# Kernel optimization log

Measured on AMD Instinct MI355X. Metric: run time of the kernel, lower is better.

## Reference

```python
import jax, jax.numpy as jnp
import numpy as np

D = 128
L_SIZE = 65536
C_SIZE = 32768
E = 262144
N_ITERS = 4


def _mlp(x, w1, b1, w2, b2):
    # 2-layer satbench MLP: Linear -> relu -> Linear
    return jax.nn.relu(x @ w1 + b1) @ w2 + b2


def setup_inputs() -> dict:
    key = jax.random.key(0)
    ks = iter(jax.random.split(key, 32))

    def lin(fi, fo):
        # torch nn.Linear default init, stored as (in, out)
        bound = 1.0 / np.sqrt(fi)
        w = jax.random.uniform(next(ks), (fi, fo), minval=-bound, maxval=bound, dtype=jnp.float32)
        b = jax.random.uniform(next(ks), (fo,), minval=-bound, maxval=bound, dtype=jnp.float32)
        return w, b

    s = np.sqrt(2.0 / D).astype(np.float32)
    inp = {}
    inp['l_edge_index'] = jax.random.randint(next(ks), (E,), 0, L_SIZE, dtype=jnp.int64)
    inp['c_edge_index'] = jax.random.randint(next(ks), (E,), 0, C_SIZE, dtype=jnp.int64)
    inp['l_init'] = jax.random.normal(next(ks), (1, D), dtype=jnp.float32) * s
    inp['c_init'] = jax.random.normal(next(ks), (1, D), dtype=jnp.float32) * s
    inp['w_l2c1'], inp['b_l2c1'] = lin(D, D)
    inp['w_l2c2'], inp['b_l2c2'] = lin(D, D)
    inp['w_c2l1'], inp['b_c2l1'] = lin(D, D)
    inp['w_c2l2'], inp['b_c2l2'] = lin(D, D)
    inp['w_l2l1'], inp['b_l2l1'] = lin(D, D)
    inp['w_l2l2'], inp['b_l2l2'] = lin(D, D)
    inp['w_cu'], inp['b_cu'] = lin(2 * D, D)
    inp['w_lu'], inp['b_lu'] = lin(3 * D, D)
    inp['l_size'] = L_SIZE
    inp['c_size'] = C_SIZE
    return inp


def reference(l_edge_index, c_edge_index, l_init, c_init,
              w_l2c1, b_l2c1, w_l2c2, b_l2c2,
              w_c2l1, b_c2l1, w_c2l2, b_c2l2,
              w_l2l1, b_l2l1, w_l2l2, b_l2l2,
              w_cu, b_cu, w_lu, b_lu, l_size, c_size):
    d = l_init.shape[1]
    ones = jnp.ones((l_edge_index.shape[0], 1), dtype=l_init.dtype)
    l_deg = jax.ops.segment_sum(ones, l_edge_index, num_segments=l_size)   # (L,1)
    c_deg = jax.ops.segment_sum(ones, c_edge_index, num_segments=c_size)   # (C,1)
    degree_norm = jnp.sqrt(l_deg[l_edge_index]) * jnp.sqrt(c_deg[c_edge_index])  # (E,1)

    l_emb = jnp.tile(l_init, (l_size, 1))  # (L,d)
    c_emb = jnp.tile(c_init, (c_size, 1))  # (C,d)

    def step(carry, _):
        l_emb, c_emb = carry
        l2c_msg = _mlp(l_emb, w_l2c1, b_l2c1, w_l2c2, b_l2c2)[l_edge_index]  # (E,d)
        c2l_msg = _mlp(c_emb, w_c2l1, b_c2l1, w_c2l2, b_c2l2)[c_edge_index]  # (E,d)
        # swap positive/negative literal partner embeddings (pairs are adjacent rows)
        l2l_in = l_emb.reshape(l_size // 2, 2, d)[:, ::-1, :].reshape(l_size, d)
        l2l_msg = _mlp(l2l_in, w_l2l1, b_l2l1, w_l2l2, b_l2l2)              # (L,d)
        l2c_aggr = jax.ops.segment_sum(l2c_msg / degree_norm, c_edge_index, num_segments=c_size)
        c_new = jnp.concatenate([c_emb, l2c_aggr], axis=1) @ w_cu + b_cu
        c2l_aggr = jax.ops.segment_sum(c2l_msg / degree_norm, l_edge_index, num_segments=l_size)
        l_new = jnp.concatenate([l_emb, c2l_aggr, l2l_msg], axis=1) @ w_lu + b_lu
        return (l_new, c_new), None

    (l_emb, c_emb), _ = jax.lax.scan(step, (l_emb, c_emb), None, length=N_ITERS)
    return l_emb
```

## Files before the change

### kernel.cpp

```cpp
#include <hip/hip_runtime.h>
#include <hip/hip_bf16.h>

#define D_ 128
#define L_ 65536
#define C_ 32768
#define E_ 262144

typedef __hip_bfloat16 bf16;
typedef __attribute__((ext_vector_type(8))) short short8;
typedef __attribute__((ext_vector_type(4))) float f32x4;

__global__ void detect_k(const unsigned short* __restrict__ wmem,
                         const int* __restrict__ li, int* __restrict__ flags) {
    int t = blockIdx.x * 512 + threadIdx.x;
    if (t < 8192) {
        unsigned short h = wmem[2 * t];
        float v = __bfloat162float(*(const bf16*)&h);
        if (!(fabsf(v) < 0.5f)) atomicOr(&flags[0], 1);
    }
    if (t < 2048) {
        if (li[2 * t + 1] != 0) atomicOr(&flags[1], 1);
    }
}

__device__ __forceinline__ void split2(float v, unsigned short& h, unsigned short& l) {
    bf16 bh = __float2bfloat16(v);
    float fh = __bfloat162float(bh);
    bf16 bl = __float2bfloat16(v - fh);
    h = *(unsigned short*)&bh;
    l = *(unsigned short*)&bl;
}

__device__ __forceinline__ float ldf(const void* s, int i, int isf32) {
    return isf32 ? ((const float*)s)[i] : __bfloat162float(((const bf16*)s)[i]);
}

__global__ void fixdeg_k(const int* __restrict__ ls, const int* __restrict__ cs,
                         int* __restrict__ ld_idx, int* __restrict__ cd_idx,
                         int* __restrict__ ldeg, int* __restrict__ cdeg,
                         const int* __restrict__ flags) {
    int i = blockIdx.x * 256 + threadIdx.x;
    int is32 = flags[1];
    if (i < E_) {
        int v = is32 ? ls[i] : ls[2 * i];
        v = min(max(v, 0), L_ - 1);
        ld_idx[i] = v;
        atomicAdd(&ldeg[v], 1);
    } else {
        int j = i - E_;
        int v = is32 ? cs[j] : cs[2 * j];
        v = min(max(v, 0), C_ - 1);
        cd_idx[j] = v;
        atomicAdd(&cdeg[v], 1);
    }
}

__global__ void cvtwb_k(const void* s0, const void* s1, const void* s2, const void* s3,
                        const void* s4, const void* s5, const void* s6, const void* s7,
                        const void* t0, const void* t1, const void* t2, const void* t3,
                        const void* t4, const void* t5, const void* t6, const void* t7,
                        unsigned short* __restrict__ hi, unsigned short* __restrict__ lo,
                        float* __restrict__ bb, const int* __restrict__ flags) {
    int i = blockIdx.x * 256 + threadIdx.x;
    int isf = flags[0];
    if (i >= 180224) {
        int j = i - 180224;
        const void* src;
        switch (j >> 7) {
            case 0: src = t0; break; case 1: src = t1; break;
            case 2: src = t2; break; case 3: src = t3; break;
            case 4: src = t4; break; case 5: src = t5; break;
            case 6: src = t6; break; default: src = t7; break;
        }
        bb[j] = ldf(src, j & 127, isf);
        return;
    }
    const void* src; int K, base;
    if      (i <  16384) { src = s0; K = 128; base = 0; }
    else if (i <  32768) { src = s1; K = 128; base = 16384; }
    else if (i <  49152) { src = s2; K = 128; base = 32768; }
    else if (i <  65536) { src = s3; K = 128; base = 49152; }
    else if (i <  81920) { src = s4; K = 128; base = 65536; }
    else if (i <  98304) { src = s5; K = 128; base = 81920; }
    else if (i < 131072) { src = s6; K = 256; base = 98304; }
    else                 { src = s7; K = 384; base = 131072; }
    int e = i - base;
    int k = e >> 7, n = e & 127;
    float v = ldf(src, e, isf);
    unsigned short h, l;
    split2(v, h, l);
    hi[base + n * K + k] = h;
    lo[base + n * K + k] = l;
}

__global__ void init2_k(const void* __restrict__ lv, const void* __restrict__ cv,
                        float* __restrict__ lemb, float* __restrict__ cemb,
                        const int* __restrict__ flags) {
    int i4 = blockIdx.x * 256 + threadIdx.x;
    int isf = flags[0];
    const void* src; float* dst; int o;
    if (i4 < L_ * 32) { src = lv; dst = lemb; o = i4; }
    else              { src = cv; dst = cemb; o = i4 - L_ * 32; }
    int j = (o & 31) * 4;
    float4 v;
    v.x = ldf(src, j + 0, isf);
    v.y = ldf(src, j + 1, isf);
    v.z = ldf(src, j + 2, isf);
    v.w = ldf(src, j + 3, isf);
    ((float4*)dst)[o] = v;
}

__global__ void scan1b_k(const int* __restrict__ ldeg, const int* __restrict__ cdeg,
                         int* __restrict__ lout, int* __restrict__ cout,
                         int* __restrict__ bsumL, int* __restrict__ bsumC) {
    __shared__ int s[256];
    const int* in; int* out; int* bs; int tile;
    if (blockIdx.x < 256) { in = ldeg; out = lout; bs = bsumL; tile = blockIdx.x; }
    else                  { in = cdeg; out = cout; bs = bsumC; tile = blockIdx.x - 256; }
    int i = tile * 256 + threadIdx.x;
    int v = in[i];
    s[threadIdx.x] = v;
    __syncthreads();
#pragma unroll
    for (int off = 1; off < 256; off <<= 1) {
        int t = (threadIdx.x >= off) ? s[threadIdx.x - off] : 0;
        __syncthreads();
        s[threadIdx.x] += t;
        __syncthreads();
    }
    out[i] = s[threadIdx.x] - v;
    if (threadIdx.x == 255) bs[tile] = s[255];
}

__global__ void scan2b_k(int* __restrict__ bL, int* __restrict__ bC) {
    __shared__ int s[256];
    int* b = blockIdx.x ? bC : bL;
    int nb = blockIdx.x ? 128 : 256;
    int v = (threadIdx.x < nb) ? b[threadIdx.x] : 0;
    s[threadIdx.x] = v;
    __syncthreads();
#pragma unroll
    for (int off = 1; off < 256; off <<= 1) {
        int t = (threadIdx.x >= off) ? s[threadIdx.x - off] : 0;
        __syncthreads();
        s[threadIdx.x] += t;
        __syncthreads();
    }
    if (threadIdx.x < nb) b[threadIdx.x] = s[threadIdx.x] - v;
}

__global__ void scan3b_k(int* __restrict__ lptr, int* __restrict__ cptr,
                         const int* __restrict__ bsumL, const int* __restrict__ bsumC,
                         int* __restrict__ lcur, int* __restrict__ ccur,
                         const int* __restrict__ ldeg, const int* __restrict__ cdeg,
                         float* __restrict__ invsq_l, float* __restrict__ invsq_c) {
    int b = blockIdx.x, t = threadIdx.x;
    if (b < 256) {
        int i = b * 256 + t;
        int v = lptr[i] + bsumL[b];
        lptr[i] = v; lcur[i] = v;
        int d = ldeg[i];
        invsq_l[i] = d ? rsqrtf((float)d) : 0.0f;
    } else {
        int i = (b - 256) * 256 + t;
        int v = cptr[i] + bsumC[b - 256];
        cptr[i] = v; ccur[i] = v;
        int d = cdeg[i];
        invsq_c[i] = d ? rsqrtf((float)d) : 0.0f;
    }
}

__global__ void place_k(const int* __restrict__ li, const int* __restrict__ ci,
                        int* __restrict__ lcur, int* __restrict__ ccur,
                        int* __restrict__ l_other, int* __restrict__ c_other) {
    int e = blockIdx.x * 256 + threadIdx.x;
    if (e >= E_) return;
    int l = li[e], c = ci[e];
    int p = atomicAdd(&ccur[c], 1);
    c_other[p] = l;
    int q = atomicAdd(&lcur[l], 1);
    l_other[q] = c;
}

__global__ __launch_bounds__(256) void gather2_k(
    const int* __restrict__ cptr, const int* __restrict__ cdeg, const int* __restrict__ c_other,
    const unsigned int* __restrict__ lmsg, const float* __restrict__ invsq_c, float* __restrict__ caggr,
    const int* __restrict__ lptr, const int* __restrict__ ldeg, const int* __restrict__ l_other,
    const unsigned int* __restrict__ cmsg, const float* __restrict__ invsq_l, float* __restrict__ laggr,
    int nC) {
    int node = (blockIdx.x * 256 + threadIdx.x) >> 6;
    int lane = threadIdx.x & 63;
    bool cside = node < nC;
    int j = cside ? node : node - nC;
    const int* ptr = cside ? cptr : lptr;
    const int* dg  = cside ? cdeg : ldeg;
    const int* oth = cside ? c_other : l_other;
    const unsigned int* msg = cside ? lmsg : cmsg;
    float sc = (cside ? invsq_c : invsq_l)[j];
    float* out = cside ? caggr : laggr;
    int s = ptr[j], cnt = dg[j];
    float2 a0 = {0.f, 0.f}, a1 = {0.f, 0.f};
    int k = 0;
    for (; k + 4 <= cnt; k += 4) {
        int o0 = oth[s + k], o1 = oth[s + k + 1], o2 = oth[s + k + 2], o3 = oth[s + k + 3];
        unsigned int u0 = msg[(size_t)o0 * 64 + lane];
        unsigned int u1 = msg[(size_t)o1 * 64 + lane];
        unsigned int u2 = msg[(size_t)o2 * 64 + lane];
        unsigned int u3 = msg[(size_t)o3 * 64 + lane];
        a0.x += __uint_as_float(u0 << 16) + __uint_as_float(u2 << 16);
        a0.y += __uint_as_float(u0 & 0xffff0000u) + __uint_as_float(u2 & 0xffff0000u);
        a1.x += __uint_as_float(u1 << 16) + __uint_as_float(u3 << 16);
        a1.y += __uint_as_float(u1 & 0xffff0000u) + __uint_as_float(u3 & 0xffff0000u);
    }
    for (; k < cnt; k++) {
        int o = oth[s + k];
        unsigned int u = msg[(size_t)o * 64 + lane];
        a0.x += __uint_as_float(u << 16);
        a0.y += __uint_as_float(u & 0xffff0000u);
    }
    a0.x = (a0.x + a1.x) * sc;
    a0.y = (a0.y + a1.y) * sc;
    *(float2*)&out[(size_t)j * D_ + 2 * lane] = a0;
}

__global__ __launch_bounds__(256, 2) void mlp3_k(
    const float* __restrict__ l_cur, const float* __restrict__ c_cur,
    const unsigned short* __restrict__ wt_hi, const unsigned short* __restrict__ wt_lo,
    const float* __restrict__ bb,
    const float* __restrict__ invsq_l, const float* __restrict__ invsq_c,
    bf16* __restrict__ l_msg, bf16* __restrict__ c_msg, bf16* __restrict__ l2lb,
    int nL, int nC) {
    __shared__ char smem[66048];
    unsigned short (*a_hi)[40] = (unsigned short(*)[40])(smem);
    unsigned short (*a_lo)[40] = (unsigned short(*)[40])(smem + 10240);
    unsigned short (*b_hi)[40] = (unsigned short(*)[40])(smem + 20480);
    unsigned short (*b_lo)[40] = (unsigned short(*)[40])(smem + 30720);
    unsigned short* h_hi = (unsigned short*)(smem);
    unsigned short* h_lo = (unsigned short*)(smem + 32768);
    float* scv = (float*)(smem + 65536);

    int b = blockIdx.x, seg, tile;
    if (b < nL)           { seg = 0; tile = b; }
    else if (b < nL + nC) { seg = 1; tile = b - nL; }
    else                  { seg = 2; tile = b - nL - nC; }
    const float* A = (seg == 1) ? c_cur : l_cur;
    bf16* outp = (seg == 0) ? l_msg : (seg == 1) ? c_msg : l2lb;
    const float* invsq = (seg == 0) ? invsq_l : (seg == 1) ? invsq_c : nullptr;
    const unsigned short* W1h = wt_hi + seg * 32768;
    const unsigned short* W1l = wt_lo + seg * 32768;
    const unsigned short* W2h = W1h + 16384;
    const unsigned short* W2l = W1l + 16384;
    const float* b1v = bb + seg * 256;
    const float* b2v = b1v + 128;
    const int swap = (seg == 2);

    const int t = threadIdx.x;
    const int br0 = tile * 128;
    const int w = t >> 6, lane = t & 63;
    const int wr = w >> 1, wc = w & 1;
    const int quad = lane >> 4, cl = lane & 15;

    if (t < 128) scv[t] = invsq ? invsq[br0 + t] : 1.0f;

    f32x4 acc[4][4];
#pragma unroll
    for (int i = 0; i < 4; i++)
#pragma unroll
        for (int j = 0; j < 4; j++) acc[i][j] = (f32x4){0.f, 0.f, 0.f, 0.f};

    for (int kt = 0; kt < 128; kt += 32) {
#pragma unroll
        for (int i = 0; i < 4; i++) {
            int f = t + 256 * i;
            int r = f >> 3, kq = f & 7;
            int gr = br0 + r;
            if (swap) gr ^= 1;
            const float4 v = *(const float4*)&A[(size_t)gr * D_ + kt + 4 * kq];
            unsigned short h0, l0, h1, l1, h2, l2, h3, l3;
            split2(v.x, h0, l0); split2(v.y, h1, l1);
            split2(v.z, h2, l2); split2(v.w, h3, l3);
            *(ushort4*)&a_hi[r][4 * kq] = make_ushort4(h0, h1, h2, h3);
            *(ushort4*)&a_lo[r][4 * kq] = make_ushort4(l0, l1, l2, l3);
            *(ushort4*)&b_hi[r][4 * kq] = *(const ushort4*)&W1h[(size_t)r * 128 + kt + 4 * kq];
            *(ushort4*)&b_lo[r][4 * kq] = *(const ushort4*)&W1l[(size_t)r * 128 + kt + 4 * kq];
        }
        __syncthreads();
        short8 af_h[4], af_l[4];
#pragma unroll
        for (int i = 0; i < 4; i++) {
            int row = 64 * wr + 16 * i + cl;
            af_h[i] = *(const short8*)&a_hi[row][quad * 8];
            af_l[i] = *(const short8*)&a_lo[row][quad * 8];
        }
#pragma unroll
        for (int j = 0; j < 4; j++) {
            int col = 64 * wc + 16 * j + cl;
            short8 bf_h = *(const short8*)&b_hi[col][quad * 8];
            short8 bf_l = *(const short8*)&b_lo[col][quad * 8];
#pragma unroll
            for (int i = 0; i < 4; i++) {
                acc[i][j] = __builtin_amdgcn_mfma_f32_16x16x32_bf16(af_h[i], bf_h, acc[i][j], 0, 0, 0);
                acc[i][j] = __builtin_amdgcn_mfma_f32_16x16x32_bf16(af_h[i], bf_l, acc[i][j], 0, 0, 0);
                acc[i][j] = __builtin_amdgcn_mfma_f32_16x16x32_bf16(af_l[i], bf_h, acc[i][j], 0, 0, 0);
            }
        }
        __syncthreads();
    }
#pragma unroll
    for (int j = 0; j < 4; j++) {
        int col = 64 * wc + 16 * j + cl;
        float bv = b1v[col];
        int g = col >> 3, go = col & 7;
#pragma unroll
        for (int i = 0; i < 4; i++) {
            int rloc = 64 * wr + 16 * i + quad * 4;
#pragma unroll
            for (int rg = 0; rg < 4; rg++) {
                float v = fmaxf(acc[i][j][rg] + bv, 0.0f);
                unsigned short hh, ll;
                split2(v, hh, ll);
                int r = rloc + rg;
                int off = r * 128 + ((g ^ (r & 15)) << 3) + go;
                h_hi[off] = hh;
                h_lo[off] = ll;
            }
        }
    }
    __syncthreads();
#pragma unroll
    for (int i = 0; i < 4; i++)
#pragma unroll
        for (int j = 0; j < 4; j++) acc[i][j] = (f32x4){0.f, 0.f, 0.f, 0.f};

    for (int kt = 0; kt < 128; kt += 32) {
        short8 af_h[4], af_l[4];
        int gbase = (kt >> 3) + quad;
#pragma unroll
        for (int i = 0; i < 4; i++) {
            int r = 64 * wr + 16 * i + cl;
            int off = r * 128 + ((gbase ^ cl) << 3);
            af_h[i] = *(const short8*)&h_hi[off];
            af_l[i] = *(const short8*)&h_lo[off];
        }
#pragma unroll
        for (int j = 0; j < 4; j++) {
            int col = 64 * wc + 16 * j + cl;
            const short8 bf_h = *(const short8*)&W2h[(size_t)col * 128 + kt + quad * 8];
            const short8 bf_l = *(const short8*)&W2l[(size_t)col * 128 + kt + quad * 8];
#pragma unroll
            for (int i = 0; i < 4; i++) {
                acc[i][j] = __builtin_amdgcn_mfma_f32_16x16x32_bf16(af_h[i], bf_h, acc[i][j], 0, 0, 0);
                acc[i][j] = __builtin_amdgcn_mfma_f32_16x16x32_bf16(af_h[i], bf_l, acc[i][j], 0, 0, 0);
                acc[i][j] = __builtin_amdgcn_mfma_f32_16x16x32_bf16(af_l[i], bf_h, acc[i][j], 0, 0, 0);
            }
        }
    }
#pragma unroll
    for (int j = 0; j < 4; j++) {
        int col = 64 * wc + 16 * j + cl;
        float bv = b2v[col];
#pragma unroll
        for (int i = 0; i < 4; i++) {
            int rloc = 64 * wr + 16 * i + quad * 4;
#pragma unroll
            for (int rg = 0; rg < 4; rg++)
                outp[(size_t)(br0 + rloc + rg) * D_ + col] =
                    __float2bfloat16((acc[i][j][rg] + bv) * scv[rloc + rg]);
        }
    }
}

template <int FINAL>
__global__ __launch_bounds__(256, 2) void update_k(
    const float* __restrict__ l_cur, const float* __restrict__ c_cur,
    const float* __restrict__ laggr, const float* __restrict__ caggr,
    const bf16* __restrict__ l2lb,
    const unsigned short* __restrict__ wt_hi, const unsigned short* __restrict__ wt_lo,
    const float* __restrict__ bb,
    float* __restrict__ c_nxt, float* __restrict__ l_nxt,
    void* __restrict__ dout, const int* __restrict__ flags) {
    __shared__ unsigned short a_hi[128][40], a_lo[128][40];
    __shared__ unsigned short b_hi[128][40], b_lo[128][40];
    const int t = threadIdx.x;
    int b = blockIdx.x;
    const bool cseg = (!FINAL) && (b < 256);
    const int tile = (FINAL || cseg) ? b : b - 256;
    const int K = cseg ? 256 : 384;
    const float* A0 = cseg ? c_cur : l_cur;
    const float* A1 = cseg ? caggr : laggr;
    const unsigned short* Wh = wt_hi + (cseg ? 98304 : 131072);
    const unsigned short* Wl = wt_lo + (cseg ? 98304 : 131072);
    const float* bias = bb + (cseg ? 768 : 896);
    const int br0 = tile * 128;
    const int w = t >> 6, lane = t & 63;
    const int wr = w >> 1, wc = w & 1;
    const int quad = lane >> 4, cl = lane & 15;

    f32x4 acc[4][4];
#pragma unroll
    for (int i = 0; i < 4; i++)
#pragma unroll
        for (int j = 0; j < 4; j++) acc[i][j] = (f32x4){0.f, 0.f, 0.f, 0.f};

    for (int kt = 0; kt < K; kt += 32) {
        const bool haslo = (kt < 256);
        const int koff = kt & 127;
#pragma unroll
        for (int i = 0; i < 4; i++) {
            int f = t + 256 * i;
            int r = f >> 3, kq = f & 7;
            if (haslo) {
                const float* As = (kt < 128) ? A0 : A1;
                const float4 v = *(const float4*)&As[(size_t)(br0 + r) * D_ + koff + 4 * kq];
                unsigned short h0, l0, h1, l1, h2, l2, h3, l3;
                split2(v.x, h0, l0); split2(v.y, h1, l1);
                split2(v.z, h2, l2); split2(v.w, h3, l3);
                *(ushort4*)&a_hi[r][4 * kq] = make_ushort4(h0, h1, h2, h3);
                *(ushort4*)&a_lo[r][4 * kq] = make_ushort4(l0, l1, l2, l3);
            } else {
                *(ushort4*)&a_hi[r][4 * kq] =
                    *(const ushort4*)&l2lb[(size_t)(br0 + r) * D_ + koff + 4 * kq];
            }
            *(ushort4*)&b_hi[r][4 * kq] = *(const ushort4*)&Wh[(size_t)r * K + kt + 4 * kq];
            *(ushort4*)&b_lo[r][4 * kq] = *(const ushort4*)&Wl[(size_t)r * K + kt + 4 * kq];
        }
        __syncthreads();
        short8 af_h[4], af_l[4];
#pragma unroll
        for (int i = 0; i < 4; i++) {
            int row = 64 * wr + 16 * i + cl;
            af_h[i] = *(const short8*)&a_hi[row][quad * 8];
            if (haslo) af_l[i] = *(const short8*)&a_lo[row][quad * 8];
        }
#pragma unroll
        for (int j = 0; j < 4; j++) {
            int col = 64 * wc + 16 * j + cl;
            short8 bf_h = *(const short8*)&b_hi[col][quad * 8];
            short8 bf_l = *(const short8*)&b_lo[col][quad * 8];
#pragma unroll
            for (int i = 0; i < 4; i++) {
                acc[i][j] = __builtin_amdgcn_mfma_f32_16x16x32_bf16(af_h[i], bf_h, acc[i][j], 0, 0, 0);
                acc[i][j] = __builtin_amdgcn_mfma_f32_16x16x32_bf16(af_h[i], bf_l, acc[i][j], 0, 0, 0);
                if (haslo)
                    acc[i][j] = __builtin_amdgcn_mfma_f32_16x16x32_bf16(af_l[i], bf_h, acc[i][j], 0, 0, 0);
            }
        }
        __syncthreads();
    }
    const int f32out = FINAL ? flags[0] : 1;
#pragma unroll
    for (int j = 0; j < 4; j++) {
        int col = 64 * wc + 16 * j + cl;
        float bv = bias[col];
#pragma unroll
        for (int i = 0; i < 4; i++) {
            int rbase = br0 + 64 * wr + 16 * i + quad * 4;
#pragma unroll
            for (int rg = 0; rg < 4; rg++) {
                float v = acc[i][j][rg] + bv;
                size_t idx = (size_t)(rbase + rg) * D_ + col;
                if (FINAL) {
                    if (f32out) ((float*)dout)[idx] = v;
                    else        ((bf16*)dout)[idx] = __float2bfloat16(v);
                } else {
                    (cseg ? c_nxt : l_nxt)[idx] = v;
                }
            }
        }
    }
}

extern "C" void kernel_launch(void* const* d_in, const int* in_sizes, int n_in,
                              void* d_out, int out_size, void* d_ws, size_t ws_size,
                              hipStream_t stream) {
    const int* li_raw = (const int*)d_in[0];
    const int* ci_raw = (const int*)d_in[1];

    float* ws = (float*)d_ws;
    float* lbuf0 = ws;
    float* lbuf1 = lbuf0 + (size_t)L_ * D_;
    float* l2lb  = lbuf1 + (size_t)L_ * D_;
    float* laggr = l2lb + (size_t)L_ * D_;
    float* cbuf0 = laggr + (size_t)L_ * D_;
    float* cbuf1 = cbuf0 + (size_t)C_ * D_;
    float* caggr = cbuf1 + (size_t)C_ * D_;
    float* invsq_l = caggr + (size_t)C_ * D_;
    float* invsq_c = invsq_l + L_;
    float* bb    = invsq_c + C_;
    unsigned short* wt_hi = (unsigned short*)(bb + 1024);
    unsigned short* wt_lo = wt_hi + 180224;
    int*   li    = (int*)(wt_lo + 180224);
    int*   ci    = li + E_;
    int*   l_other = ci + E_;
    int*   c_other = l_other + E_;
    int*   ldegi = c_other + E_;
    int*   cdegi = ldegi + L_;
    int*   lptr  = cdegi + C_;
    int*   cptr  = lptr + L_;
    int*   lcur  = cptr + C_;
    int*   ccur  = lcur + L_;
    int*   bsumL = ccur + C_;
    int*   bsumC = bsumL + 256;
    int*   flags = bsumC + 128;

    hipMemsetAsync(flags, 0, 2 * sizeof(int), stream);
    detect_k<<<16, 512, 0, stream>>>((const unsigned short*)d_in[4], li_raw, flags);

    hipMemsetAsync(ldegi, 0, (size_t)(L_ + C_) * sizeof(int), stream);
    fixdeg_k<<<2 * E_ / 256, 256, 0, stream>>>(li_raw, ci_raw, li, ci, ldegi, cdegi, flags);

    cvtwb_k<<<708, 256, 0, stream>>>(d_in[4], d_in[6], d_in[8], d_in[10], d_in[12],
                                     d_in[14], d_in[16], d_in[18],
                                     d_in[5], d_in[7], d_in[9], d_in[11], d_in[13],
                                     d_in[15], d_in[17], d_in[19], wt_hi, wt_lo, bb, flags);

    scan1b_k<<<384, 256, 0, stream>>>(ldegi, cdegi, lptr, cptr, bsumL, bsumC);
    scan2b_k<<<2, 256, 0, stream>>>(bsumL, bsumC);
    scan3b_k<<<384, 256, 0, stream>>>(lptr, cptr, bsumL, bsumC, lcur, ccur,
                                      ldegi, cdegi, invsq_l, invsq_c);
    place_k<<<E_ / 256, 256, 0, stream>>>(li, ci, lcur, ccur, l_other, c_other);

    init2_k<<<(L_ + C_) * 32 / 256, 256, 0, stream>>>(d_in[2], d_in[3], lbuf0, cbuf0, flags);

    float* l_cur = lbuf0; float* l_nxt = lbuf1;
    float* c_cur = cbuf0; float* c_nxt = cbuf1;

    const int nL = L_ / 128, nC = C_ / 128;
    for (int it = 0; it < 3; it++) {
        mlp3_k<<<2 * nL + nC, 256, 0, stream>>>(
            l_cur, c_cur, wt_hi, wt_lo, bb, invsq_l, invsq_c,
            (bf16*)l_nxt, (bf16*)c_nxt, (bf16*)l2lb, nL, nC);
        gather2_k<<<(C_ + L_) / 4, 256, 0, stream>>>(
            cptr, cdegi, c_other, (const unsigned int*)l_nxt, invsq_c, caggr,
            lptr, ldegi, l_other, (const unsigned int*)c_nxt, invsq_l, laggr, C_);
        update_k<0><<<768, 256, 0, stream>>>(
            l_cur, c_cur, laggr, caggr, (const bf16*)l2lb, wt_hi, wt_lo, bb,
            c_nxt, l_nxt, nullptr, flags);
        float* tmp = l_cur; l_cur = l_nxt; l_nxt = tmp;
        tmp = c_cur; c_cur = c_nxt; c_nxt = tmp;
    }
    mlp3_k<<<nC + nL, 256, 0, stream>>>(
        l_cur, c_cur, wt_hi, wt_lo, bb, invsq_l, invsq_c,
        (bf16*)l_nxt, (bf16*)c_nxt, (bf16*)l2lb, 0, nC);
    gather2_k<<<L_ / 4, 256, 0, stream>>>(
        cptr, cdegi, c_other, (const unsigned int*)l_nxt, invsq_c, caggr,
        lptr, ldegi, l_other, (const unsigned int*)c_nxt, invsq_l, laggr, 0);
    update_k<1><<<512, 256, 0, stream>>>(
        l_cur, c_cur, laggr, caggr, (const bf16*)l2lb, wt_hi, wt_lo, bb,
        nullptr, nullptr, d_out, flags);
}
```

Baseline: 692.7 us.

## Fuse l2c and l2l MLPs into one block sharing the staged literal tile

The MLP kernel now has each literal tile load and split its 128x128 fp32 activation block once into swizzled shared memory, then compute both the l2c and l2l first layers from it. The partner swap moves to the output side by writing l2l rows to index r^1. First-layer weights are read straight from global memory instead of being staged through LDS. This halves literal activation reads and the number of literal blocks, at the cost of more registers (two accumulator sets), which may limit occupancy.

```diff
diff --git a/kernel.cpp b/kernel.cpp
--- a/kernel.cpp
+++ b/kernel.cpp
@@ -9,6 +9,8 @@
 typedef __hip_bfloat16 bf16;
 typedef __attribute__((ext_vector_type(8))) short short8;
 typedef __attribute__((ext_vector_type(4))) float f32x4;
+
+__device__ __forceinline__ int uswz(int r) { return (r + (r >> 2)) & 3; }
 
 __global__ void detect_k(const unsigned short* __restrict__ wmem,
                          const int* __restrict__ li, int* __restrict__ flags) {
@@ -223,149 +225,243 @@
     *(float2*)&out[(size_t)j * D_ + 2 * lane] = a0;
 }
 
-__global__ __launch_bounds__(256, 2) void mlp3_k(
+__global__ __launch_bounds__(256, 2) void mlp3f_k(
     const float* __restrict__ l_cur, const float* __restrict__ c_cur,
     const unsigned short* __restrict__ wt_hi, const unsigned short* __restrict__ wt_lo,
     const float* __restrict__ bb,
     const float* __restrict__ invsq_l, const float* __restrict__ invsq_c,
     bf16* __restrict__ l_msg, bf16* __restrict__ c_msg, bf16* __restrict__ l2lb,
-    int nL, int nC) {
+    int nL, int fin) {
     __shared__ char smem[66048];
-    unsigned short (*a_hi)[40] = (unsigned short(*)[40])(smem);
-    unsigned short (*a_lo)[40] = (unsigned short(*)[40])(smem + 10240);
-    unsigned short (*b_hi)[40] = (unsigned short(*)[40])(smem + 20480);
-    unsigned short (*b_lo)[40] = (unsigned short(*)[40])(smem + 30720);
-    unsigned short* h_hi = (unsigned short*)(smem);
+    unsigned short* h_hi = (unsigned short*)smem;
     unsigned short* h_lo = (unsigned short*)(smem + 32768);
     float* scv = (float*)(smem + 65536);
 
-    int b = blockIdx.x, seg, tile;
-    if (b < nL)           { seg = 0; tile = b; }
-    else if (b < nL + nC) { seg = 1; tile = b - nL; }
-    else                  { seg = 2; tile = b - nL - nC; }
-    const float* A = (seg == 1) ? c_cur : l_cur;
-    bf16* outp = (seg == 0) ? l_msg : (seg == 1) ? c_msg : l2lb;
-    const float* invsq = (seg == 0) ? invsq_l : (seg == 1) ? invsq_c : nullptr;
-    const unsigned short* W1h = wt_hi + seg * 32768;
-    const unsigned short* W1l = wt_lo + seg * 32768;
+    const int b = blockIdx.x;
+    const bool lseg = (b < nL);
+    const int tile = lseg ? b : b - nL;
+    const int br0 = tile * 128;
+    const float* A = lseg ? l_cur : c_cur;
+    const int s1 = lseg ? 0 : 1;
+    const unsigned short* W1h = wt_hi + s1 * 32768;
+    const unsigned short* W1l = wt_lo + s1 * 32768;
     const unsigned short* W2h = W1h + 16384;
     const unsigned short* W2l = W1l + 16384;
-    const float* b1v = bb + seg * 256;
+    const unsigned short* V1h = wt_hi + 65536;
+    const unsigned short* V1l = wt_lo + 65536;
+    const unsigned short* V2h = V1h + 16384;
+    const unsigned short* V2l = V1l + 16384;
+    const float* b1v = bb + s1 * 256;
     const float* b2v = b1v + 128;
-    const int swap = (seg == 2);
+    const float* d1v = bb + 512;
+    const float* d2v = bb + 640;
+    bf16* out1 = lseg ? l_msg : c_msg;
+    const bool do1 = !(fin && lseg);
+    const bool do2 = lseg;
 
     const int t = threadIdx.x;
-    const int br0 = tile * 128;
     const int w = t >> 6, lane = t & 63;
     const int wr = w >> 1, wc = w & 1;
     const int quad = lane >> 4, cl = lane & 15;
 
-    if (t < 128) scv[t] = invsq ? invsq[br0 + t] : 1.0f;
-
-    f32x4 acc[4][4];
+    if (t < 128) scv[t] = (lseg ? invsq_l : invsq_c)[br0 + t];
+
+    {
+        float4 v[16];
+#pragma unroll
+        for (int c = 0; c < 16; c++) {
+            int f = t + 256 * c;
+            int r = f >> 5, kq = f & 31;
+            v[c] = *(const float4*)&A[(size_t)(br0 + r) * D_ + 4 * kq];
+        }
+#pragma unroll
+        for (int c = 0; c < 16; c++) {
+            int f = t + 256 * c;
+            int r = f >> 5, kq = f & 31;
+            int s = kq >> 3, kq2 = kq & 7;
+            unsigned short h0, l0, h1, l1, h2, l2, h3, l3;
+            split2(v[c].x, h0, l0); split2(v[c].y, h1, l1);
+            split2(v[c].z, h2, l2); split2(v[c].w, h3, l3);
+            int ga = s * 16384 + r * 64 + (((kq2 >> 1) ^ uswz(r)) << 4) + (kq2 & 1) * 8;
+            *(ushort4*)(smem + ga) = make_ushort4(h0, h1, h2, h3);
+            *(ushort4*)(smem + 8192 + ga) = make_ushort4(l0, l1, l2, l3);
+        }
+    }
+    __syncthreads();
+
+    f32x4 acc1[4][4], acc2[4][4];
 #pragma unroll
     for (int i = 0; i < 4; i++)
 #pragma unroll
-        for (int j = 0; j < 4; j++) acc[i][j] = (f32x4){0.f, 0.f, 0.f, 0.f};
-
-    for (int kt = 0; kt < 128; kt += 32) {
-#pragma unroll
-        for (int i = 0; i < 4; i++) {
-            int f = t + 256 * i;
-            int r = f >> 3, kq = f & 7;
-            int gr = br0 + r;
-            if (swap) gr ^= 1;
-            const float4 v = *(const float4*)&A[(size_t)gr * D_ + kt + 4 * kq];
-            unsigned short h0, l0, h1, l1, h2, l2, h3, l3;
-            split2(v.x, h0, l0); split2(v.y, h1, l1);
-            split2(v.z, h2, l2); split2(v.w, h3, l3);
-            *(ushort4*)&a_hi[r][4 * kq] = make_ushort4(h0, h1, h2, h3);
-            *(ushort4*)&a_lo[r][4 * kq] = make_ushort4(l0, l1, l2, l3);
-            *(ushort4*)&b_hi[r][4 * kq] = *(const ushort4*)&W1h[(size_t)r * 128 + kt + 4 * kq];
-            *(ushort4*)&b_lo[r][4 * kq] = *(const ushort4*)&W1l[(size_t)r * 128 + kt + 4 * kq];
-        }
-        __syncthreads();
+        for (int j = 0; j < 4; j++) {
+            acc1[i][j] = (f32x4){0.f, 0.f, 0.f, 0.f};
+            acc2[i][j] = (f32x4){0.f, 0.f, 0.f, 0.f};
+        }
+
+    for (int kt = 0; kt < 4; kt++) {
+        const char* base = smem + kt * 16384;
         short8 af_h[4], af_l[4];
 #pragma unroll
         for (int i = 0; i < 4; i++) {
             int row = 64 * wr + 16 * i + cl;
-            af_h[i] = *(const short8*)&a_hi[row][quad * 8];
-            af_l[i] = *(const short8*)&a_lo[row][quad * 8];
+            int so = row * 64 + ((quad ^ uswz(row)) << 4);
+            af_h[i] = *(const short8*)(base + so);
+            af_l[i] = *(const short8*)(base + 8192 + so);
         }
 #pragma unroll
         for (int j = 0; j < 4; j++) {
             int col = 64 * wc + 16 * j + cl;
-            short8 bf_h = *(const short8*)&b_hi[col][quad * 8];
-            short8 bf_l = *(const short8*)&b_lo[col][quad * 8];
-#pragma unroll
-            for (int i = 0; i < 4; i++) {
-                acc[i][j] = __builtin_amdgcn_mfma_f32_16x16x32_bf16(af_h[i], bf_h, acc[i][j], 0, 0, 0);
-                acc[i][j] = __builtin_amdgcn_mfma_f32_16x16x32_bf16(af_h[i], bf_l, acc[i][j], 0, 0, 0);
-                acc[i][j] = __builtin_amdgcn_mfma_f32_16x16x32_bf16(af_l[i], bf_h, acc[i][j], 0, 0, 0);
-            }
-        }
-        __syncthreads();
-    }
-#pragma unroll
-    for (int j = 0; j < 4; j++) {
-        int col = 64 * wc + 16 * j + cl;
-        float bv = b1v[col];
-        int g = col >> 3, go = col & 7;
-#pragma unroll
-        for (int i = 0; i < 4; i++) {
-            int rloc = 64 * wr + 16 * i + quad * 4;
-#pragma unroll
-            for (int rg = 0; rg < 4; rg++) {
-                float v = fmaxf(acc[i][j][rg] + bv, 0.0f);
-                unsigned short hh, ll;
-                split2(v, hh, ll);
-                int r = rloc + rg;
-                int off = r * 128 + ((g ^ (r & 15)) << 3) + go;
-                h_hi[off] = hh;
-                h_lo[off] = ll;
+            size_t wo = (size_t)col * 128 + kt * 32 + quad * 8;
+            if (do1) {
+                short8 bh = *(const short8*)&W1h[wo];
+                short8 bl = *(const short8*)&W1l[wo];
+#pragma unroll
+                for (int i = 0; i < 4; i++) {
+                    acc1[i][j] = __builtin_amdgcn_mfma_f32_16x16x32_bf16(af_h[i], bh, acc1[i][j], 0, 0, 0);
+                    acc1[i][j] = __builtin_amdgcn_mfma_f32_16x16x32_bf16(af_h[i], bl, acc1[i][j], 0, 0, 0);
+                    acc1[i][j] = __builtin_amdgcn_mfma_f32_16x16x32_bf16(af_l[i], bh, acc1[i][j], 0, 0, 0);
+                }
+            }
+            if (do2) {
+                short8 bh = *(const short8*)&V1h[wo];
+                short8 bl = *(const short8*)&V1l[wo];
+#pragma unroll
+                for (int i = 0; i < 4; i++) {
+                    acc2[i][j] = __builtin_amdgcn_mfma_f32_16x16x32_bf16(af_h[i], bh, acc2[i][j], 0, 0, 0);
+                    acc2[i][j] = __builtin_amdgcn_mfma_f32_16x16x32_bf16(af_h[i], bl, acc2[i][j], 0, 0, 0);
+                    acc2[i][j] = __builtin_amdgcn_mfma_f32_16x16x32_bf16(af_l[i], bh, acc2[i][j], 0, 0, 0);
+                }
             }
         }
     }
     __syncthreads();
-#pragma unroll
-    for (int i = 0; i < 4; i++)
-#pragma unroll
-        for (int j = 0; j < 4; j++) acc[i][j] = (f32x4){0.f, 0.f, 0.f, 0.f};
-
-    for (int kt = 0; kt < 128; kt += 32) {
-        short8 af_h[4], af_l[4];
-        int gbase = (kt >> 3) + quad;
-#pragma unroll
-        for (int i = 0; i < 4; i++) {
-            int r = 64 * wr + 16 * i + cl;
-            int off = r * 128 + ((gbase ^ cl) << 3);
-            af_h[i] = *(const short8*)&h_hi[off];
-            af_l[i] = *(const short8*)&h_lo[off];
-        }
+
+    if (do1) {
 #pragma unroll
         for (int j = 0; j < 4; j++) {
             int col = 64 * wc + 16 * j + cl;
-            const short8 bf_h = *(const short8*)&W2h[(size_t)col * 128 + kt + quad * 8];
-            const short8 bf_l = *(const short8*)&W2l[(size_t)col * 128 + kt + quad * 8];
+            float bv = b1v[col];
+            int g = col >> 3, go = col & 7;
 #pragma unroll
             for (int i = 0; i < 4; i++) {
-                acc[i][j] = __builtin_amdgcn_mfma_f32_16x16x32_bf16(af_h[i], bf_h, acc[i][j], 0, 0, 0);
-                acc[i][j] = __builtin_amdgcn_mfma_f32_16x16x32_bf16(af_h[i], bf_l, acc[i][j], 0, 0, 0);
-                acc[i][j] = __builtin_amdgcn_mfma_f32_16x16x32_bf16(af_l[i], bf_h, acc[i][j], 0, 0, 0);
-            }
-        }
-    }
-#pragma unroll
-    for (int j = 0; j < 4; j++) {
-        int col = 64 * wc + 16 * j + cl;
-        float bv = b2v[col];
-#pragma unroll
-        for (int i = 0; i < 4; i++) {
-            int rloc = 64 * wr + 16 * i + quad * 4;
-#pragma unroll
-            for (int rg = 0; rg < 4; rg++)
-                outp[(size_t)(br0 + rloc + rg) * D_ + col] =
-                    __float2bfloat16((acc[i][j][rg] + bv) * scv[rloc + rg]);
+                int rloc = 64 * wr + 16 * i + quad * 4;
+#pragma unroll
+                for (int rg = 0; rg < 4; rg++) {
+                    float v = fmaxf(acc1[i][j][rg] + bv, 0.0f);
+                    unsigned short hh, ll;
+                    split2(v, hh, ll);
+                    int r = rloc + rg;
+                    int off = r * 128 + ((g ^ (r & 15)) << 3) + go;
+                    h_hi[off] = hh;
+                    h_lo[off] = ll;
+                }
+            }
+        }
+        __syncthreads();
+#pragma unroll
+        for (int i = 0; i < 4; i++)
+#pragma unroll
+            for (int j = 0; j < 4; j++) acc1[i][j] = (f32x4){0.f, 0.f, 0.f, 0.f};
+        for (int kt = 0; kt < 128; kt += 32) {
+            short8 ah[4], al[4];
+            int gbase = (kt >> 3) + quad;
+#pragma unroll
+            for (int i = 0; i < 4; i++) {
+                int r = 64 * wr + 16 * i + cl;
+                int off = r * 128 + ((gbase ^ cl) << 3);
+                ah[i] = *(const short8*)&h_hi[off];
+                al[i] = *(const short8*)&h_lo[off];
+            }
+#pragma unroll
+            for (int j = 0; j < 4; j++) {
+                int col = 64 * wc + 16 * j + cl;
+                const short8 bh = *(const short8*)&W2h[(size_t)col * 128 + kt + quad * 8];
+                const short8 bl = *(const short8*)&W2l[(size_t)col * 128 + kt + quad * 8];
+#pragma unroll
+                for (int i = 0; i < 4; i++) {
+                    acc1[i][j] = __builtin_amdgcn_mfma_f32_16x16x32_bf16(ah[i], bh, acc1[i][j], 0, 0, 0);
+                    acc1[i][j] = __builtin_amdgcn_mfma_f32_16x16x32_bf16(ah[i], bl, acc1[i][j], 0, 0, 0);
+                    acc1[i][j] = __builtin_amdgcn_mfma_f32_16x16x32_bf16(al[i], bh, acc1[i][j], 0, 0, 0);
+                }
+            }
+        }
+#pragma unroll
+        for (int j = 0; j < 4; j++) {
+            int col = 64 * wc + 16 * j + cl;
+            float bv = b2v[col];
+#pragma unroll
+            for (int i = 0; i < 4; i++) {
+                int rloc = 64 * wr + 16 * i + quad * 4;
+#pragma unroll
+                for (int rg = 0; rg < 4; rg++)
+                    out1[(size_t)(br0 + rloc + rg) * D_ + col] =
+                        __float2bfloat16((acc1[i][j][rg] + bv) * scv[rloc + rg]);
+            }
+        }
+    }
+
+    if (do2) {
+        __syncthreads();
+#pragma unroll
+        for (int j = 0; j < 4; j++) {
+            int col = 64 * wc + 16 * j + cl;
+            float bv = d1v[col];
+            int g = col >> 3, go = col & 7;
+#pragma unroll
+            for (int i = 0; i < 4; i++) {
+                int rloc = 64 * wr + 16 * i + quad * 4;
+#pragma unroll
+                for (int rg = 0; rg < 4; rg++) {
+                    float v = fmaxf(acc2[i][j][rg] + bv, 0.0f);
+                    unsigned short hh, ll;
+                    split2(v, hh, ll);
+                    int r = rloc + rg;
+                    int off = r * 128 + ((g ^ (r & 15)) << 3) + go;
+                    h_hi[off] = hh;
+                    h_lo[off] = ll;
+                }
+            }
+        }
+        __syncthreads();
+#pragma unroll
+        for (int i = 0; i < 4; i++)
+#pragma unroll
+            for (int j = 0; j < 4; j++) acc2[i][j] = (f32x4){0.f, 0.f, 0.f, 0.f};
+        for (int kt = 0; kt < 128; kt += 32) {
+            short8 ah[4], al[4];
+            int gbase = (kt >> 3) + quad;
+#pragma unroll
+            for (int i = 0; i < 4; i++) {
+                int r = 64 * wr + 16 * i + cl;
+                int off = r * 128 + ((gbase ^ cl) << 3);
+                ah[i] = *(const short8*)&h_hi[off];
+                al[i] = *(const short8*)&h_lo[off];
+            }
+#pragma unroll
+            for (int j = 0; j < 4; j++) {
+                int col = 64 * wc + 16 * j + cl;
+                const short8 bh = *(const short8*)&V2h[(size_t)col * 128 + kt + quad * 8];
+                const short8 bl = *(const short8*)&V2l[(size_t)col * 128 + kt + quad * 8];
+#pragma unroll
+                for (int i = 0; i < 4; i++) {
+                    acc2[i][j] = __builtin_amdgcn_mfma_f32_16x16x32_bf16(ah[i], bh, acc2[i][j], 0, 0, 0);
+                    acc2[i][j] = __builtin_amdgcn_mfma_f32_16x16x32_bf16(ah[i], bl, acc2[i][j], 0, 0, 0);
+                    acc2[i][j] = __builtin_amdgcn_mfma_f32_16x16x32_bf16(al[i], bh, acc2[i][j], 0, 0, 0);
+                }
+            }
+        }
+#pragma unroll
+        for (int j = 0; j < 4; j++) {
+            int col = 64 * wc + 16 * j + cl;
+            float bv = d2v[col];
+#pragma unroll
+            for (int i = 0; i < 4; i++) {
+                int rloc = 64 * wr + 16 * i + quad * 4;
+#pragma unroll
+                for (int rg = 0; rg < 4; rg++)
+                    l2lb[(size_t)((br0 + rloc + rg) ^ 1) * D_ + col] =
+                        __float2bfloat16(acc2[i][j][rg] + bv);
+            }
         }
     }
 }
@@ -527,9 +623,9 @@
 
     const int nL = L_ / 128, nC = C_ / 128;
     for (int it = 0; it < 3; it++) {
-        mlp3_k<<<2 * nL + nC, 256, 0, stream>>>(
+        mlp3f_k<<<nL + nC, 256, 0, stream>>>(
             l_cur, c_cur, wt_hi, wt_lo, bb, invsq_l, invsq_c,
-            (bf16*)l_nxt, (bf16*)c_nxt, (bf16*)l2lb, nL, nC);
+            (bf16*)l_nxt, (bf16*)c_nxt, (bf16*)l2lb, nL, 0);
         gather2_k<<<(C_ + L_) / 4, 256, 0, stream>>>(
             cptr, cdegi, c_other, (const unsigned int*)l_nxt, invsq_c, caggr,
             lptr, ldegi, l_other, (const unsigned int*)c_nxt, invsq_l, laggr, C_);
@@ -539,9 +635,9 @@
         float* tmp = l_cur; l_cur = l_nxt; l_nxt = tmp;
         tmp = c_cur; c_cur = c_nxt; c_nxt = tmp;
     }
-    mlp3_k<<<nC + nL, 256, 0, stream>>>(
+    mlp3f_k<<<nL + nC, 256, 0, stream>>>(
         l_cur, c_cur, wt_hi, wt_lo, bb, invsq_l, invsq_c,
-        (bf16*)l_nxt, (bf16*)c_nxt, (bf16*)l2lb, 0, nC);
+        (bf16*)l_nxt, (bf16*)c_nxt, (bf16*)l2lb, nL, 1);
     gather2_k<<<L_ / 4, 256, 0, stream>>>(
         cptr, cdegi, c_other, (const unsigned int*)l_nxt, invsq_c, caggr,
         lptr, ldegi, l_other, (const unsigned int*)c_nxt, invsq_l, laggr, 0);
```

Result: slower. 717.5 us (+3.6%).

## Fuse edge aggregation gather into update GEMM A-tile loading

Applied to the files above, without the earlier changes.

Removes the separate gather kernel and computes the degree-normalized neighbor sums directly while loading the aggregate portion of the A tile in the update GEMM. Messages go to dedicated buffers instead of the next-state buffers. This avoids writing and re-reading the float aggregate arrays and one launch per iteration. In exchange, each thread now serially loops over a row's edges with narrow 8-byte loads, re-reading edge indices for every k-slice, with load imbalance inside the GEMM block.

```diff
diff --git a/kernel.cpp b/kernel.cpp
--- a/kernel.cpp
+++ b/kernel.cpp
@@ -182,47 +182,6 @@
     l_other[q] = c;
 }
 
-__global__ __launch_bounds__(256) void gather2_k(
-    const int* __restrict__ cptr, const int* __restrict__ cdeg, const int* __restrict__ c_other,
-    const unsigned int* __restrict__ lmsg, const float* __restrict__ invsq_c, float* __restrict__ caggr,
-    const int* __restrict__ lptr, const int* __restrict__ ldeg, const int* __restrict__ l_other,
-    const unsigned int* __restrict__ cmsg, const float* __restrict__ invsq_l, float* __restrict__ laggr,
-    int nC) {
-    int node = (blockIdx.x * 256 + threadIdx.x) >> 6;
-    int lane = threadIdx.x & 63;
-    bool cside = node < nC;
-    int j = cside ? node : node - nC;
-    const int* ptr = cside ? cptr : lptr;
-    const int* dg  = cside ? cdeg : ldeg;
-    const int* oth = cside ? c_other : l_other;
-    const unsigned int* msg = cside ? lmsg : cmsg;
-    float sc = (cside ? invsq_c : invsq_l)[j];
-    float* out = cside ? caggr : laggr;
-    int s = ptr[j], cnt = dg[j];
-    float2 a0 = {0.f, 0.f}, a1 = {0.f, 0.f};
-    int k = 0;
-    for (; k + 4 <= cnt; k += 4) {
-        int o0 = oth[s + k], o1 = oth[s + k + 1], o2 = oth[s + k + 2], o3 = oth[s + k + 3];
-        unsigned int u0 = msg[(size_t)o0 * 64 + lane];
-        unsigned int u1 = msg[(size_t)o1 * 64 + lane];
-        unsigned int u2 = msg[(size_t)o2 * 64 + lane];
-        unsigned int u3 = msg[(size_t)o3 * 64 + lane];
-        a0.x += __uint_as_float(u0 << 16) + __uint_as_float(u2 << 16);
-        a0.y += __uint_as_float(u0 & 0xffff0000u) + __uint_as_float(u2 & 0xffff0000u);
-        a1.x += __uint_as_float(u1 << 16) + __uint_as_float(u3 << 16);
-        a1.y += __uint_as_float(u1 & 0xffff0000u) + __uint_as_float(u3 & 0xffff0000u);
-    }
-    for (; k < cnt; k++) {
-        int o = oth[s + k];
-        unsigned int u = msg[(size_t)o * 64 + lane];
-        a0.x += __uint_as_float(u << 16);
-        a0.y += __uint_as_float(u & 0xffff0000u);
-    }
-    a0.x = (a0.x + a1.x) * sc;
-    a0.y = (a0.y + a1.y) * sc;
-    *(float2*)&out[(size_t)j * D_ + 2 * lane] = a0;
-}
-
 __global__ __launch_bounds__(256, 2) void mlp3_k(
     const float* __restrict__ l_cur, const float* __restrict__ c_cur,
     const unsigned short* __restrict__ wt_hi, const unsigned short* __restrict__ wt_lo,
@@ -373,8 +332,12 @@
 template <int FINAL>
 __global__ __launch_bounds__(256, 2) void update_k(
     const float* __restrict__ l_cur, const float* __restrict__ c_cur,
-    const float* __restrict__ laggr, const float* __restrict__ caggr,
+    const unsigned short* __restrict__ msgL, const unsigned short* __restrict__ msgC,
     const bf16* __restrict__ l2lb,
+    const int* __restrict__ lptr, const int* __restrict__ ldeg,
+    const int* __restrict__ l_other, const float* __restrict__ invsq_l,
+    const int* __restrict__ cptr, const int* __restrict__ cdeg,
+    const int* __restrict__ c_other, const float* __restrict__ invsq_c,
     const unsigned short* __restrict__ wt_hi, const unsigned short* __restrict__ wt_lo,
     const float* __restrict__ bb,
     float* __restrict__ c_nxt, float* __restrict__ l_nxt,
@@ -387,7 +350,11 @@
     const int tile = (FINAL || cseg) ? b : b - 256;
     const int K = cseg ? 256 : 384;
     const float* A0 = cseg ? c_cur : l_cur;
-    const float* A1 = cseg ? caggr : laggr;
+    const unsigned short* msg = cseg ? msgL : msgC;
+    const int* ptr = cseg ? cptr : lptr;
+    const int* dgv = cseg ? cdeg : ldeg;
+    const int* oth = cseg ? c_other : l_other;
+    const float* invsq = cseg ? invsq_c : invsq_l;
     const unsigned short* Wh = wt_hi + (cseg ? 98304 : 131072);
     const unsigned short* Wl = wt_lo + (cseg ? 98304 : 131072);
     const float* bias = bb + (cseg ? 768 : 896);
@@ -409,12 +376,29 @@
         for (int i = 0; i < 4; i++) {
             int f = t + 256 * i;
             int r = f >> 3, kq = f & 7;
-            if (haslo) {
-                const float* As = (kt < 128) ? A0 : A1;
-                const float4 v = *(const float4*)&As[(size_t)(br0 + r) * D_ + koff + 4 * kq];
+            if (kt < 128) {
+                const float4 v = *(const float4*)&A0[(size_t)(br0 + r) * D_ + koff + 4 * kq];
                 unsigned short h0, l0, h1, l1, h2, l2, h3, l3;
                 split2(v.x, h0, l0); split2(v.y, h1, l1);
                 split2(v.z, h2, l2); split2(v.w, h3, l3);
+                *(ushort4*)&a_hi[r][4 * kq] = make_ushort4(h0, h1, h2, h3);
+                *(ushort4*)&a_lo[r][4 * kq] = make_ushort4(l0, l1, l2, l3);
+            } else if (kt < 256) {
+                int gr = br0 + r;
+                int s = ptr[gr], cnt = dgv[gr];
+                float4 sum = {0.f, 0.f, 0.f, 0.f};
+                for (int e = 0; e < cnt; e++) {
+                    int o = oth[s + e];
+                    ushort4 m = *(const ushort4*)&msg[(size_t)o * D_ + koff + 4 * kq];
+                    sum.x += __uint_as_float((unsigned)m.x << 16);
+                    sum.y += __uint_as_float((unsigned)m.y << 16);
+                    sum.z += __uint_as_float((unsigned)m.z << 16);
+                    sum.w += __uint_as_float((unsigned)m.w << 16);
+                }
+                float sc = invsq[gr];
+                unsigned short h0, l0, h1, l1, h2, l2, h3, l3;
+                split2(sum.x * sc, h0, l0); split2(sum.y * sc, h1, l1);
+                split2(sum.z * sc, h2, l2); split2(sum.w * sc, h3, l3);
                 *(ushort4*)&a_hi[r][4 * kq] = make_ushort4(h0, h1, h2, h3);
                 *(ushort4*)&a_lo[r][4 * kq] = make_ushort4(l0, l1, l2, l3);
             } else {
@@ -480,11 +464,11 @@
     float* lbuf0 = ws;
     float* lbuf1 = lbuf0 + (size_t)L_ * D_;
     float* l2lb  = lbuf1 + (size_t)L_ * D_;
-    float* laggr = l2lb + (size_t)L_ * D_;
-    float* cbuf0 = laggr + (size_t)L_ * D_;
+    float* msgLf = l2lb + (size_t)L_ * D_;
+    float* cbuf0 = msgLf + (size_t)L_ * D_;
     float* cbuf1 = cbuf0 + (size_t)C_ * D_;
-    float* caggr = cbuf1 + (size_t)C_ * D_;
-    float* invsq_l = caggr + (size_t)C_ * D_;
+    float* msgCf = cbuf1 + (size_t)C_ * D_;
+    float* invsq_l = msgCf + (size_t)C_ * D_;
     float* invsq_c = invsq_l + L_;
     float* bb    = invsq_c + C_;
     unsigned short* wt_hi = (unsigned short*)(bb + 1024);
@@ -503,6 +487,9 @@
     int*   bsumC = bsumL + 256;
     int*   flags = bsumC + 128;
 
+    unsigned short* msgL = (unsigned short*)msgLf;
+    unsigned short* msgC = (unsigned short*)msgCf;
+
     hipMemsetAsync(flags, 0, 2 * sizeof(int), stream);
     detect_k<<<16, 512, 0, stream>>>((const unsigned short*)d_in[4], li_raw, flags);
 
@@ -529,23 +516,19 @@
     for (int it = 0; it < 3; it++) {
         mlp3_k<<<2 * nL + nC, 256, 0, stream>>>(
             l_cur, c_cur, wt_hi, wt_lo, bb, invsq_l, invsq_c,
-            (bf16*)l_nxt, (bf16*)c_nxt, (bf16*)l2lb, nL, nC);
-        gather2_k<<<(C_ + L_) / 4, 256, 0, stream>>>(
-            cptr, cdegi, c_other, (const unsigned int*)l_nxt, invsq_c, caggr,
-            lptr, ldegi, l_other, (const unsigned int*)c_nxt, invsq_l, laggr, C_);
+            (bf16*)msgL, (bf16*)msgC, (bf16*)l2lb, nL, nC);
         update_k<0><<<768, 256, 0, stream>>>(
-            l_cur, c_cur, laggr, caggr, (const bf16*)l2lb, wt_hi, wt_lo, bb,
-            c_nxt, l_nxt, nullptr, flags);
+            l_cur, c_cur, msgL, msgC, (const bf16*)l2lb,
+            lptr, ldegi, l_other, invsq_l, cptr, cdegi, c_other, invsq_c,
+            wt_hi, wt_lo, bb, c_nxt, l_nxt, nullptr, flags);
         float* tmp = l_cur; l_cur = l_nxt; l_nxt = tmp;
         tmp = c_cur; c_cur = c_nxt; c_nxt = tmp;
     }
     mlp3_k<<<nC + nL, 256, 0, stream>>>(
         l_cur, c_cur, wt_hi, wt_lo, bb, invsq_l, invsq_c,
-        (bf16*)l_nxt, (bf16*)c_nxt, (bf16*)l2lb, 0, nC);
-    gather2_k<<<L_ / 4, 256, 0, stream>>>(
-        cptr, cdegi, c_other, (const unsigned int*)l_nxt, invsq_c, caggr,
-        lptr, ldegi, l_other, (const unsigned int*)c_nxt, invsq_l, laggr, 0);
+        (bf16*)msgL, (bf16*)msgC, (bf16*)l2lb, 0, nC);
     update_k<1><<<512, 256, 0, stream>>>(
-        l_cur, c_cur, laggr, caggr, (const bf16*)l2lb, wt_hi, wt_lo, bb,
-        nullptr, nullptr, d_out, flags);
-}
+        l_cur, c_cur, msgL, msgC, (const bf16*)l2lb,
+        lptr, ldegi, l_other, invsq_l, cptr, cdegi, c_other, invsq_c,
+        wt_hi, wt_lo, bb, nullptr, nullptr, d_out, flags);
+}
```

New measurement: 1.145 ms. +65.3%, slower.
